# Optimization experiments

Measured on AMD Instinct MI355X. Metric: run time of the kernel, lower is better.

Reference implementation:

```python
import jax, jax.numpy as jnp
import numpy as np

H = W = 20
NVARS = 4          # n_predictor_vars
NK = 12            # n_conv2d_kernels
NF = NK + NVARS + 1  # 17 augmented channels (conv + original + time)
SIGLEN = NF + NF * NF  # 306, depth-2 signature length
T_END = 1.0        # self.T in the module


def setup_inputs() -> dict:
    key = jax.random.key(0)
    ks = jax.random.split(key, 8)
    B, T = 64, 96
    x = jax.random.normal(ks[0], (B, T, NVARS, H, W), dtype=jnp.float32)
    conv_w = jax.random.normal(ks[1], (NK, NVARS, 3, 3), dtype=jnp.float32) * 0.1
    conv_b = jax.random.normal(ks[2], (NK,), dtype=jnp.float32) * 0.01
    d_in = SIGLEN * H * W  # 122400

    def lin(k, fan_in, fan_out):
        return jax.random.normal(k, (fan_in, fan_out), dtype=jnp.float32) / np.float32(np.sqrt(fan_in))

    w1, b1 = lin(ks[3], d_in, 32), jnp.zeros((32,), jnp.float32)
    w2, b2 = lin(ks[4], 32, 32), jnp.zeros((32,), jnp.float32)
    w3, b3 = lin(ks[5], 32, 32), jnp.zeros((32,), jnp.float32)
    w4, b4 = lin(ks[6], 32, 1), jnp.zeros((1,), jnp.float32)
    return {"x": x, "conv_w": conv_w, "conv_b": conv_b,
            "w1": w1, "b1": b1, "w2": w2, "b2": b2,
            "w3": w3, "b3": b3, "w4": w4, "b4": b4}


def reference(x, conv_w, conv_b, w1, b1, w2, b2, w3, b3, w4, b4):
    B, T = x.shape[0], x.shape[1]
    # Batched conv over all timesteps at once (the torch code loops over t).
    xi = x.reshape(B * T, NVARS, H, W)
    y = jax.lax.conv_general_dilated(
        xi, conv_w, window_strides=(1, 1), padding='SAME',
        dimension_numbers=('NCHW', 'OIHW', 'NCHW'))
    y = y + conv_b[None, :, None, None]
    y = y.reshape(B, T, NK, H, W)
    # Dropout3d is identity in eval mode.
    # Augment: [conv features, original values, time channel] along channel dim.
    tch = jnp.linspace(0.0, T_END, T, dtype=x.dtype).reshape(1, T, 1, 1, 1)
    tch = jnp.broadcast_to(tch, (B, T, 1, H, W))
    feat = jnp.concatenate([y, x, tch], axis=2)        # (B, T, NF, H, W)
    path = jnp.transpose(feat, (0, 3, 4, 1, 2))        # (B, H, W, T, NF)
    # Depth-2 path signature (Chen closed form):
    # level1 = sum dx; level2 = sum_{i<j} dx_i (x) dx_j + 0.5 sum_i dx_i (x) dx_i
    dx = path[..., 1:, :] - path[..., :-1, :]          # (B,H,W,T-1,NF)
    csum = jnp.cumsum(dx, axis=-2)                     # inclusive prefix sums
    lvl1 = csum[..., -1, :]                            # (B,H,W,NF)
    # (exclusive prefix) + 0.5*dx = csum - 0.5*dx -> single contracted einsum
    lvl2 = jnp.einsum('bhwti,bhwtj->bhwij', csum - 0.5 * dx, dx)
    sig = jnp.concatenate([lvl1, lvl2.reshape(B, H, W, NF * NF)], axis=-1)  # (B,H,W,306)
    flat = sig.reshape(B, H * W * SIGLEN)
    h = jax.nn.relu(flat @ w1 + b1)
    h = jax.nn.relu(h @ w2 + b2)
    h = jax.nn.relu(h @ w3 + b3)
    return h @ w4 + b4                                 # (B, 1)
```

## Files before the change

kernel.cpp:

```cpp
#include <hip/hip_runtime.h>

#define HH 20
#define WW 20
#define TT 96
#define BB 64
#define SIG 306
#define NFC 17
#define TSTRIDE 260
#define CHUNK 16
#define NCHUNK 6
#define XT 199
#define KTOT 122400
#define KSLAB 120
#define NSLAB 4
#define NKBLK 255
#define LDT 66

typedef float float4u __attribute__((ext_vector_type(4), aligned(4)));

__global__ __launch_bounds__(256) void sig_kernel(
    const float* __restrict__ x,
    const float* __restrict__ cw,
    float* __restrict__ sig)
{
  __shared__ __align__(16) float feat[15 * TSTRIDE + 256 + 8];
  __shared__ __align__(16) float xs[CHUNK * XT];

  const int tid = threadIdx.x;
  const int blk = blockIdx.x;
  const int b = blk / 25;
  const int tile = blk % 25;
  const int th4 = (tile / 5) * 4, tw4 = (tile % 5) * 4;
  const float* xb0 = x + (size_t)b * TT * 1600;

  int g_off[9], l_off[9];
  #pragma unroll
  for (int r = 0; r < 9; r++) {
    int idx = r * 256 + tid;
    int t = idx / 144, q = idx % 144;
    int ci = q / 36, pos = q % 36, row = pos / 6, col = pos % 6;
    int gr = th4 - 1 + row, gc = tw4 - 1 + col;
    bool valid = (gr >= 0 && gr < HH && gc >= 0 && gc < WW);
    g_off[r] = valid ? (t * 1600 + ci * 400 + gr * WW + gc) : -1;
    l_off[r] = t * XT + ci * 48 + row * 8 + col;
  }

  const int cpix = tid >> 4, ctt = tid & 15;
  const int cpy = cpix >> 2, cpx = cpix & 3;

  const int p2 = tid >> 4;
  const int rr = tid & 15, it = rr >> 2, jt = rr & 3;
  const int i0 = it * 4, j0 = jt * 4;

  float accv[4][4];
  float f0a[4], f0b[4], pa[4], pb[4], fsum[4];
  #pragma unroll
  for (int i = 0; i < 4; i++) {
    #pragma unroll
    for (int j = 0; j < 4; j++) accv[i][j] = 0.f;
  }

  auto stage = [&](int chunk) {
    const float* xbc = xb0 + (size_t)chunk * CHUNK * 1600;
    float rg[9];
    #pragma unroll
    for (int r = 0; r < 9; r++)
      rg[r] = (g_off[r] >= 0) ? xbc[g_off[r]] : 0.f;
    #pragma unroll
    for (int r = 0; r < 9; r++) xs[l_off[r]] = rg[r];
  };

  auto conv = [&]() {
    float win[4][9];
    const int wb2 = ctt * XT;
    #pragma unroll
    for (int ci = 0; ci < 4; ci++)
      #pragma unroll
      for (int dy = 0; dy < 3; dy++)
        #pragma unroll
        for (int dxx = 0; dxx < 3; dxx++)
          win[ci][dy * 3 + dxx] = xs[wb2 + ci * 48 + (cpy + dy) * 8 + (cpx + dxx)];

    float fk[12];
    #pragma unroll
    for (int k = 0; k < 12; k++) {
      float a = 0.f;
      #pragma unroll
      for (int ci = 0; ci < 4; ci++) {
        #pragma unroll
        for (int p = 0; p < 9; p++)
          a += win[ci][p] * cw[k * 36 + ci * 9 + p];
      }
      fk[k] = a;
    }
    float* fr = &feat[ctt * TSTRIDE + cpix * 16];
    *reinterpret_cast<float4*>(fr + 0)  = make_float4(fk[0], fk[1], fk[2], fk[3]);
    *reinterpret_cast<float4*>(fr + 4)  = make_float4(fk[4], fk[5], fk[6], fk[7]);
    *reinterpret_cast<float4*>(fr + 8)  = make_float4(fk[8], fk[9], fk[10], fk[11]);
    *reinterpret_cast<float4*>(fr + 12) = make_float4(win[0][4], win[1][4], win[2][4], win[3][4]);
  };

  auto p2step = [&](int tt) {
    const float* row = &feat[tt * TSTRIDE + p2 * 16];
    const float4 a4 = *reinterpret_cast<const float4*>(row + i0);
    const float4 b4 = *reinterpret_cast<const float4*>(row + j0);
    float fa[4] = {a4.x, a4.y, a4.z, a4.w};
    float fb[4] = {b4.x, b4.y, b4.z, b4.w};
    float sa[4], db[4];
    #pragma unroll
    for (int i = 0; i < 4; i++) { sa[i] = fa[i] + pa[i]; db[i] = fb[i] - pb[i]; }
    #pragma unroll
    for (int i = 0; i < 4; i++)
      #pragma unroll
      for (int j = 0; j < 4; j++) accv[i][j] += sa[i] * db[j];
    #pragma unroll
    for (int i = 0; i < 4; i++) { fsum[i] += fa[i]; pa[i] = fa[i]; pb[i] = fb[i]; }
  };

  stage(0);
  __syncthreads();
  conv();
  __syncthreads();
  {
    const float* r0 = &feat[p2 * 16];
    const float4 a4 = *reinterpret_cast<const float4*>(r0 + i0);
    const float4 b4 = *reinterpret_cast<const float4*>(r0 + j0);
    f0a[0] = a4.x; f0a[1] = a4.y; f0a[2] = a4.z; f0a[3] = a4.w;
    f0b[0] = b4.x; f0b[1] = b4.y; f0b[2] = b4.z; f0b[3] = b4.w;
    #pragma unroll
    for (int i = 0; i < 4; i++) { pa[i] = f0a[i]; pb[i] = f0b[i]; fsum[i] = f0a[i]; }
  }
  #pragma unroll
  for (int tt = 1; tt < CHUNK; tt++) p2step(tt);

  for (int chunk = 1; chunk < NCHUNK; chunk++) {
    __syncthreads();
    stage(chunk);
    __syncthreads();
    conv();
    __syncthreads();
    #pragma unroll
    for (int tt = 0; tt < CHUNK; tt++) p2step(tt);
  }

  {
    const int ph = th4 + (p2 >> 2), pw = tw4 + (p2 & 3);
    float* sb = sig + (size_t)b * KTOT + (size_t)(ph * WW + pw) * SIG;
    float lv1b[4];
    #pragma unroll
    for (int j = 0; j < 4; j++) lv1b[j] = pb[j] - f0b[j];
    #pragma unroll
    for (int ii = 0; ii < 4; ii++) {
      float4u v;
      #pragma unroll
      for (int jj = 0; jj < 4; jj++)
        v[jj] = 0.5f * accv[ii][jj] - f0a[ii] * lv1b[jj];
      *reinterpret_cast<float4u*>(sb + NFC + (i0 + ii) * NFC + j0) = v;
    }
    if (jt == 0) {
      #pragma unroll
      for (int ii = 0; ii < 4; ii++) {
        const int c = i0 + ii;
        const float f0 = f0a[ii], f95 = pa[ii], fs = fsum[ii];
        sb[c] = f95 - f0;
        sb[NFC + c * NFC + 16] = (fs - 95.5f * f0 - 0.5f * f95) * (1.f / 95.f);
        sb[NFC + 16 * NFC + c] = (95.5f * f95 + 0.5f * f0 - fs) * (1.f / 95.f);
      }
      if (it == 0) { sb[16] = 1.0f; sb[NFC + 16 * NFC + 16] = 0.5f; }
    }
  }
}

template<bool ATOMIC>
__global__ __launch_bounds__(256) void mlp1_gemm(
    const float* __restrict__ sig, const float* __restrict__ w1,
    float* __restrict__ part)
{
  __shared__ __align__(16) float ldsT[KSLAB * LDT];
  __shared__ __align__(16) float wls[KSLAB * 32];
  const int tid = threadIdx.x;
  const int n = tid & 31, bq = tid >> 5;
  const int k0 = blockIdx.x * (KSLAB * NSLAB);

  float a8[8];
  #pragma unroll
  for (int i = 0; i < 8; i++) a8[i] = 0.f;

  for (int s = 0; s < NSLAB; s++) {
    const int ks = k0 + s * KSLAB;
    __syncthreads();
    #pragma unroll
    for (int r = 0; r < 30; r++) {
      int idx = r * 256 + tid;
      int b = idx / KSLAB, kk = idx % KSLAB;
      ldsT[kk * LDT + b] = sig[(size_t)b * KTOT + ks + kk];
    }
    #pragma unroll
    for (int r = 0; r < 15; r++) {
      int idx = r * 256 + tid;
      wls[idx] = w1[(size_t)ks * 32 + idx];
    }
    __syncthreads();

    #pragma unroll 4
    for (int kk = 0; kk < KSLAB; kk++) {
      const float w = wls[kk * 32 + n];
      const float4 s0 = *reinterpret_cast<const float4*>(&ldsT[kk * LDT + bq * 8]);
      const float4 s1 = *reinterpret_cast<const float4*>(&ldsT[kk * LDT + bq * 8 + 4]);
      a8[0] += s0.x * w; a8[1] += s0.y * w; a8[2] += s0.z * w; a8[3] += s0.w * w;
      a8[4] += s1.x * w; a8[5] += s1.y * w; a8[6] += s1.z * w; a8[7] += s1.w * w;
    }
  }

  if (ATOMIC) {
    #pragma unroll
    for (int i = 0; i < 8; i++)
      atomicAdd(&part[(bq * 8 + i) * 32 + n], a8[i]);
  } else {
    const size_t pb = (size_t)blockIdx.x * (BB * 32);
    #pragma unroll
    for (int i = 0; i < 8; i++)
      part[pb + (bq * 8 + i) * 32 + n] = a8[i];
  }
}

__global__ __launch_bounds__(256) void mlp_tail(
    const float* __restrict__ part, int npart, const float* __restrict__ b1,
    const float* __restrict__ w2, const float* __restrict__ b2,
    const float* __restrict__ w3, const float* __restrict__ b3,
    const float* __restrict__ w4, const float* __restrict__ b4,
    float* __restrict__ out)
{
  __shared__ float red[8][33];
  const int tid = threadIdx.x;
  const int n = tid & 31;
  const int s = tid >> 5;
  const int b = blockIdx.x;

  float sum = 0.f;
  #pragma unroll 8
  for (int p = s; p < npart; p += 8)
    sum += part[(size_t)p * (BB * 32) + b * 32 + n];
  red[s][n] = sum;
  __syncthreads();

  if (tid < 32) {
    float acc = red[0][n];
    #pragma unroll
    for (int q = 1; q < 8; q++) acc += red[q][n];

    float h = fmaxf(acc + b1[n], 0.f);

    float v = b2[n];
    #pragma unroll
    for (int k = 0; k < 32; k++)
      v += __shfl(h, k, 64) * w2[k * 32 + n];
    h = fmaxf(v, 0.f);

    v = b3[n];
    #pragma unroll
    for (int k = 0; k < 32; k++)
      v += __shfl(h, k, 64) * w3[k * 32 + n];
    h = fmaxf(v, 0.f);

    float p = h * w4[n];
    #pragma unroll
    for (int o = 16; o >= 1; o >>= 1) p += __shfl_xor(p, o, 64);
    if (n == 0) out[b] = p + b4[0];
  }
}

extern "C" void kernel_launch(void* const* d_in, const int* in_sizes, int n_in,
                              void* d_out, int out_size, void* d_ws, size_t ws_size,
                              hipStream_t stream) {
  const float* x  = (const float*)d_in[0];
  const float* cw = (const float*)d_in[1];
  const float* w1 = (const float*)d_in[3];
  const float* b1 = (const float*)d_in[4];
  const float* w2 = (const float*)d_in[5];
  const float* b2 = (const float*)d_in[6];
  const float* w3 = (const float*)d_in[7];
  const float* b3 = (const float*)d_in[8];
  const float* w4 = (const float*)d_in[9];
  const float* b4 = (const float*)d_in[10];
  float* out = (float*)d_out;

  const size_t sig_bytes  = (size_t)BB * KTOT * sizeof(float);
  const size_t part_bytes = (size_t)NKBLK * BB * 32 * sizeof(float);
  float* sigm = (float*)d_ws;

  sig_kernel<<<dim3(1600), dim3(256), 0, stream>>>(x, cw, sigm);

  if (ws_size >= sig_bytes + part_bytes) {
    float* part = (float*)((char*)d_ws + sig_bytes);
    mlp1_gemm<false><<<dim3(NKBLK), dim3(256), 0, stream>>>(sigm, w1, part);
    mlp_tail<<<dim3(64), dim3(256), 0, stream>>>(part, NKBLK, b1, w2, b2, w3, b3, w4, b4, out);
  } else {
    float* acc = (float*)((char*)d_ws + sig_bytes);
    hipMemsetAsync(acc, 0, BB * 32 * sizeof(float), stream);
    mlp1_gemm<true><<<dim3(NKBLK), dim3(256), 0, stream>>>(sigm, w1, acc);
    mlp_tail<<<dim3(64), dim3(256), 0, stream>>>(acc, 1, b1, w2, b2, w3, b3, w4, b4, out);
  }
}
```

Baseline: 255.2 us.

## Prefetch next chunk into registers in signature and GEMM kernels; halve slabs per block

Both kernels now issue the global loads for the next chunk or slab into registers before computing on the current one, then write them to shared memory afterwards. The aim is to hide global-load latency behind the conv and GEMM work instead of stalling on load-then-sync. The GEMM also halves the slabs per block (NSLAB 4→2), which doubles the block count and the partial sums to reduce. The register prefetch (rA[30], rW[15]) raises register pressure and may lower occupancy.

```diff
diff --git a/kernel.cpp b/kernel.cpp
--- a/kernel.cpp
+++ b/kernel.cpp
@@ -12,8 +12,8 @@
 #define XT 199
 #define KTOT 122400
 #define KSLAB 120
-#define NSLAB 4
-#define NKBLK 255
+#define NSLAB 2
+#define NKBLK 510
 #define LDT 66
 
 typedef float float4u __attribute__((ext_vector_type(4), aligned(4)));
@@ -54,18 +54,20 @@
 
   float accv[4][4];
   float f0a[4], f0b[4], pa[4], pb[4], fsum[4];
+  float rg[9];
   #pragma unroll
   for (int i = 0; i < 4; i++) {
     #pragma unroll
     for (int j = 0; j < 4; j++) accv[i][j] = 0.f;
   }
 
-  auto stage = [&](int chunk) {
+  auto loadrg = [&](int chunk) {
     const float* xbc = xb0 + (size_t)chunk * CHUNK * 1600;
-    float rg[9];
     #pragma unroll
     for (int r = 0; r < 9; r++)
       rg[r] = (g_off[r] >= 0) ? xbc[g_off[r]] : 0.f;
+  };
+  auto writexs = [&]() {
     #pragma unroll
     for (int r = 0; r < 9; r++) xs[l_off[r]] = rg[r];
   };
@@ -117,9 +119,11 @@
     for (int i = 0; i < 4; i++) { fsum[i] += fa[i]; pa[i] = fa[i]; pb[i] = fb[i]; }
   };
 
-  stage(0);
+  loadrg(0);
+  writexs();
   __syncthreads();
   conv();
+  loadrg(1);
   __syncthreads();
   {
     const float* r0 = &feat[p2 * 16];
@@ -134,10 +138,10 @@
   for (int tt = 1; tt < CHUNK; tt++) p2step(tt);
 
   for (int chunk = 1; chunk < NCHUNK; chunk++) {
-    __syncthreads();
-    stage(chunk);
+    writexs();
     __syncthreads();
     conv();
+    if (chunk < NCHUNK - 1) loadrg(chunk + 1);
     __syncthreads();
     #pragma unroll
     for (int tt = 0; tt < CHUNK; tt++) p2step(tt);
@@ -186,21 +190,34 @@
   #pragma unroll
   for (int i = 0; i < 8; i++) a8[i] = 0.f;
 
-  for (int s = 0; s < NSLAB; s++) {
+  float rA[30], rW[15];
+  auto loadslab = [&](int s) {
     const int ks = k0 + s * KSLAB;
-    __syncthreads();
     #pragma unroll
     for (int r = 0; r < 30; r++) {
       int idx = r * 256 + tid;
       int b = idx / KSLAB, kk = idx % KSLAB;
-      ldsT[kk * LDT + b] = sig[(size_t)b * KTOT + ks + kk];
-    }
-    #pragma unroll
-    for (int r = 0; r < 15; r++) {
+      rA[r] = sig[(size_t)b * KTOT + ks + kk];
+    }
+    #pragma unroll
+    for (int r = 0; r < 15; r++)
+      rW[r] = w1[(size_t)ks * 32 + r * 256 + tid];
+  };
+
+  loadslab(0);
+  for (int s = 0; s < NSLAB; s++) {
+    if (s) __syncthreads();
+    #pragma unroll
+    for (int r = 0; r < 30; r++) {
       int idx = r * 256 + tid;
-      wls[idx] = w1[(size_t)ks * 32 + idx];
-    }
+      int b = idx / KSLAB, kk = idx % KSLAB;
+      ldsT[kk * LDT + b] = rA[r];
+    }
+    #pragma unroll
+    for (int r = 0; r < 15; r++)
+      wls[r * 256 + tid] = rW[r];
     __syncthreads();
+    if (s + 1 < NSLAB) loadslab(s + 1);
 
     #pragma unroll 4
     for (int kk = 0; kk < KSLAB; kk++) {
```

Measured after the change: 224.0 us. 1.14x faster.
